# Performance work log

Hardware: AMD Instinct MI355X
Metric: run time of the kernel (lower is better)

Reference implementation:

```python
import jax, jax.numpy as jnp
import numpy as np
from jax.ops import segment_sum, segment_max

N, E = 50000, 800000
F_IN, H, C = 256, 4, 64
HID_LIN, OUT = 128, 16
K = 10
NEG_SLOPE = 0.2


def setup_inputs() -> dict:
    key = jax.random.key(0)
    ks = jax.random.split(key, 16)
    g = lambda k, shape, fan: jax.random.normal(k, shape, jnp.float32) * (1.0 / np.sqrt(fan))
    x = jax.random.normal(ks[0], (N, F_IN), jnp.float32)
    edge_index = jax.random.randint(ks[1], (2, E), 0, N, jnp.int64)
    # conv1: in=F_IN -> H*C, concat=True
    W1 = g(ks[2], (H * C, F_IN), F_IN)
    att_s1 = g(ks[3], (1, H, C), C)
    att_d1 = g(ks[4], (1, H, C), C)
    b1 = jnp.zeros((H * C,), jnp.float32)
    # conv2: in=H*C -> C, concat=False
    W2 = g(ks[5], (H * C, H * C), H * C)
    att_s2 = g(ks[6], (1, H, C), C)
    att_d2 = g(ks[7], (1, H, C), C)
    b2 = jnp.zeros((C,), jnp.float32)
    # linear head: C -> HID_LIN -> OUT
    Wl1 = g(ks[8], (HID_LIN, C), C)
    bl1 = jnp.zeros((HID_LIN,), jnp.float32)
    Wl2 = g(ks[9], (OUT, HID_LIN), HID_LIN)
    bl2 = jnp.zeros((OUT,), jnp.float32)
    return dict(x=x, W1=W1, att_s1=att_s1, att_d1=att_d1, b1=b1,
                W2=W2, att_s2=att_s2, att_d2=att_d2, b2=b2,
                Wl1=Wl1, bl1=bl1, Wl2=Wl2, bl2=bl2, edge_index=edge_index)


def gat_conv(x, edge_index, W, att_s, att_d, bias, concat):
    src, dst = edge_index[0], edge_index[1]
    n = x.shape[0]
    xl = (x @ W.T).reshape(n, H, C)              # [N,H,C]
    a_s = jnp.sum(xl * att_s, axis=-1)           # [N,H]
    a_d = jnp.sum(xl * att_d, axis=-1)           # [N,H]
    alpha = jax.nn.leaky_relu(a_s[src] + a_d[dst], NEG_SLOPE)  # [E,H]

    # per-(dst,head) top-k mask via sort-by-segment (rank within neighborhood)
    e = alpha.shape[0]
    counts = segment_sum(jnp.ones((e,), jnp.int32), dst, num_segments=n)
    start = jnp.cumsum(counts) - counts          # segment start offsets

    def head_mask(a):
        order = jnp.lexsort((-a, dst))           # sort by dst asc, alpha desc
        rank = jnp.arange(e) - start[dst[order]]
        return jnp.zeros((e,), bool).at[order].set(rank < K)

    mask = jax.vmap(head_mask, in_axes=1, out_axes=1)(alpha)  # [E,H]

    # segment softmax over destination with top-k mask (masked -> -inf)
    neg_inf = jnp.finfo(alpha.dtype).min
    a_masked = jnp.where(mask, alpha, neg_inf)
    m = segment_max(a_masked, dst, num_segments=n)            # [N,H]
    ex = jnp.where(mask, jnp.exp(alpha - m[dst]), 0.0)        # alpha<=m on kept edges
    denom = segment_sum(ex, dst, num_segments=n)              # [N,H]
    att = ex / jnp.where(denom[dst] > 0, denom[dst], 1.0)     # [E,H]

    # message + scatter-add aggregation
    out = segment_sum(att[:, :, None] * xl[src], dst, num_segments=n)  # [N,H,C]
    out = out.reshape(n, H * C) if concat else out.mean(axis=1)
    return out + bias


def reference(x, W1, att_s1, att_d1, b1, W2, att_s2, att_d2, b2,
              Wl1, bl1, Wl2, bl2, edge_index):
    h = gat_conv(x, edge_index, W1, att_s1, att_d1, b1, concat=True)
    h = gat_conv(h, edge_index, W2, att_s2, att_d2, b2, concat=False)
    h = jax.nn.relu(h @ Wl1.T + bl1)             # dropout is identity in eval
    return h @ Wl2.T + bl2
```

## Files before the change

kernel.cpp:

```cpp
#include <hip/hip_runtime.h>
#include <math.h>

#define F_IN 256
#define HC   256
#define H_   4
#define C_   64
#define KTOP 10
#define NEG_SLOPE 0.2f

#define BM 128
#define BN 128
#define BK 16
#define LDP (BM + 4)
__global__ __launch_bounds__(256) void gemm_nt(const float* __restrict__ A,
                                               const float* __restrict__ B,
                                               float* __restrict__ Cc,
                                               int M, int K, int No) {
  __shared__ float As[BK][LDP];
  __shared__ float Bs[BK][LDP];
  const int bm = blockIdx.x * BM;
  const int bn = blockIdx.y * BN;
  const int tid = threadIdx.x;
  const int tx = tid & 15, ty = tid >> 4;
  const int lrow = tid >> 1;
  const int lk   = (tid & 1) << 3;
  const bool arow_ok = (bm + lrow < M);
  const float* aptr = A + (size_t)(bm + lrow) * K + lk;
  const float* bptr = B + (size_t)(bn + lrow) * K + lk;
  float acc[8][8] = {};
  for (int k0 = 0; k0 < K; k0 += BK) {
    float4 a0 = make_float4(0.f, 0.f, 0.f, 0.f), a1 = a0;
    if (arow_ok) {
      const float* ap = aptr + k0;
      a0 = *(const float4*)ap;
      a1 = *(const float4*)(ap + 4);
    }
    const float* bp = bptr + k0;
    float4 b0 = *(const float4*)bp;
    float4 b1 = *(const float4*)(bp + 4);
    __syncthreads();
    As[lk + 0][lrow] = a0.x; As[lk + 1][lrow] = a0.y; As[lk + 2][lrow] = a0.z; As[lk + 3][lrow] = a0.w;
    As[lk + 4][lrow] = a1.x; As[lk + 5][lrow] = a1.y; As[lk + 6][lrow] = a1.z; As[lk + 7][lrow] = a1.w;
    Bs[lk + 0][lrow] = b0.x; Bs[lk + 1][lrow] = b0.y; Bs[lk + 2][lrow] = b0.z; Bs[lk + 3][lrow] = b0.w;
    Bs[lk + 4][lrow] = b1.x; Bs[lk + 5][lrow] = b1.y; Bs[lk + 6][lrow] = b1.z; Bs[lk + 7][lrow] = b1.w;
    __syncthreads();
#pragma unroll
    for (int kk = 0; kk < BK; ++kk) {
      float a[8];
      *(float4*)&a[0] = *(const float4*)&As[kk][ty * 8];
      *(float4*)&a[4] = *(const float4*)&As[kk][ty * 8 + 4];
      {
        float4 bv = *(const float4*)&Bs[kk][tx * 4];
#pragma unroll
        for (int i = 0; i < 8; ++i) {
          acc[i][0] += a[i] * bv.x; acc[i][1] += a[i] * bv.y;
          acc[i][2] += a[i] * bv.z; acc[i][3] += a[i] * bv.w;
        }
      }
      {
        float4 bv = *(const float4*)&Bs[kk][64 + tx * 4];
#pragma unroll
        for (int i = 0; i < 8; ++i) {
          acc[i][4] += a[i] * bv.x; acc[i][5] += a[i] * bv.y;
          acc[i][6] += a[i] * bv.z; acc[i][7] += a[i] * bv.w;
        }
      }
    }
  }
#pragma unroll
  for (int i = 0; i < 8; ++i) {
    int r = bm + ty * 8 + i;
    if (r < M) {
      float* cp = Cc + (size_t)r * No + bn;
      *(float4*)(cp + tx * 4) = make_float4(acc[i][0], acc[i][1], acc[i][2], acc[i][3]);
      *(float4*)(cp + 64 + tx * 4) = make_float4(acc[i][4], acc[i][5], acc[i][6], acc[i][7]);
    }
  }
}

__global__ __launch_bounds__(256) void gemm_bias_relu(const float* __restrict__ A,
                                                      const float* __restrict__ B,
                                                      const float* __restrict__ bias,
                                                      float* __restrict__ Cc,
                                                      int M, int K, int No) {
  __shared__ float As[BK][LDP];
  __shared__ float Bs[BK][LDP];
  const int bm = blockIdx.x * BM;
  const int bn = blockIdx.y * BN;
  const int tid = threadIdx.x;
  const int tx = tid & 15, ty = tid >> 4;
  const int lrow = tid >> 1;
  const int lk   = (tid & 1) << 3;
  const bool arow_ok = (bm + lrow < M);
  const bool brow_ok = (bn + lrow < No);
  const float* aptr = A + (size_t)(bm + lrow) * K + lk;
  const float* bptr = B + (size_t)(bn + lrow) * K + lk;
  float acc[8][8] = {};
  for (int k0 = 0; k0 < K; k0 += BK) {
    float4 a0 = make_float4(0.f, 0.f, 0.f, 0.f), a1 = a0, b0 = a0, b1 = a0;
    if (arow_ok) {
      const float* ap = aptr + k0;
      a0 = *(const float4*)ap;
      a1 = *(const float4*)(ap + 4);
    }
    if (brow_ok) {
      const float* bp = bptr + k0;
      b0 = *(const float4*)bp;
      b1 = *(const float4*)(bp + 4);
    }
    __syncthreads();
    As[lk + 0][lrow] = a0.x; As[lk + 1][lrow] = a0.y; As[lk + 2][lrow] = a0.z; As[lk + 3][lrow] = a0.w;
    As[lk + 4][lrow] = a1.x; As[lk + 5][lrow] = a1.y; As[lk + 6][lrow] = a1.z; As[lk + 7][lrow] = a1.w;
    Bs[lk + 0][lrow] = b0.x; Bs[lk + 1][lrow] = b0.y; Bs[lk + 2][lrow] = b0.z; Bs[lk + 3][lrow] = b0.w;
    Bs[lk + 4][lrow] = b1.x; Bs[lk + 5][lrow] = b1.y; Bs[lk + 6][lrow] = b1.z; Bs[lk + 7][lrow] = b1.w;
    __syncthreads();
#pragma unroll
    for (int kk = 0; kk < BK; ++kk) {
      float a[8];
      *(float4*)&a[0] = *(const float4*)&As[kk][ty * 8];
      *(float4*)&a[4] = *(const float4*)&As[kk][ty * 8 + 4];
      {
        float4 bv = *(const float4*)&Bs[kk][tx * 4];
#pragma unroll
        for (int i = 0; i < 8; ++i) {
          acc[i][0] += a[i] * bv.x; acc[i][1] += a[i] * bv.y;
          acc[i][2] += a[i] * bv.z; acc[i][3] += a[i] * bv.w;
        }
      }
      {
        float4 bv = *(const float4*)&Bs[kk][64 + tx * 4];
#pragma unroll
        for (int i = 0; i < 8; ++i) {
          acc[i][4] += a[i] * bv.x; acc[i][5] += a[i] * bv.y;
          acc[i][6] += a[i] * bv.z; acc[i][7] += a[i] * bv.w;
        }
      }
    }
  }
#pragma unroll
  for (int i = 0; i < 8; ++i) {
    int r = bm + ty * 8 + i;
    if (r < M) {
      float* cp = Cc + (size_t)r * No + bn;
#pragma unroll
      for (int j = 0; j < 4; ++j) {
        int col = tx * 4 + j;
        cp[col] = fmaxf(acc[i][j] + bias[bn + col], 0.f);
      }
#pragma unroll
      for (int j = 0; j < 4; ++j) {
        int col = 64 + tx * 4 + j;
        cp[col] = fmaxf(acc[i][4 + j] + bias[bn + col], 0.f);
      }
    }
  }
}

__global__ __launch_bounds__(256) void head_out(const float* __restrict__ hid,
                                                const float* __restrict__ Wl2,
                                                const float* __restrict__ bl2,
                                                float* __restrict__ out, int n_nodes) {
  int t = blockIdx.x * 256 + threadIdx.x;
  int n = t >> 4, o = t & 15;
  if (n >= n_nodes) return;
  const float4* hp = (const float4*)(hid + (size_t)n * 128);
  const float4* wp = (const float4*)(Wl2 + (size_t)o * 128);
  float acc = bl2[o];
#pragma unroll
  for (int k = 0; k < 32; ++k) {
    float4 hv = hp[k], wv = wp[k];
    acc += hv.x * wv.x + hv.y * wv.y + hv.z * wv.z + hv.w * wv.w;
  }
  out[(size_t)n * 16 + o] = acc;
}

__global__ __launch_bounds__(256) void fold_att1(const float* __restrict__ W1,
                                                 const float* __restrict__ att_s,
                                                 const float* __restrict__ att_d,
                                                 double* __restrict__ wt) {
  int t = blockIdx.x * 256 + threadIdx.x;
  if (t >= H_ * HC) return;
  int h = t >> 8;
  int k = t & (HC - 1);
  double s = 0.0, d = 0.0;
#pragma unroll 4
  for (int c = 0; c < C_; ++c) {
    double w = (double)W1[(size_t)(h * C_ + c) * HC + k];
    s += w * (double)att_s[h * C_ + c];
    d += w * (double)att_d[h * C_ + c];
  }
  wt[(size_t)(2 * h + 0) * HC + k] = s;
  wt[(size_t)(2 * h + 1) * HC + k] = d;
}

__global__ __launch_bounds__(256) void fold_att2(const float* __restrict__ W2,
                                                 const float* __restrict__ att_s,
                                                 const float* __restrict__ att_d,
                                                 double* __restrict__ u_s,
                                                 double* __restrict__ u_d) {
  int t = blockIdx.x * 256 + threadIdx.x;
  if (t >= H_ * HC) return;
  int h = t >> 8;
  int k = t & (HC - 1);
  double s = 0.0, d = 0.0;
#pragma unroll 4
  for (int c = 0; c < C_; ++c) {
    double w = (double)W2[(size_t)(h * C_ + c) * HC + k];
    s += w * (double)att_s[h * C_ + c];
    d += w * (double)att_d[h * C_ + c];
  }
  u_s[t] = s;
  u_d[t] = d;
}

__global__ __launch_bounds__(256) void fold_vv(const float* __restrict__ W1,
                                               const double* __restrict__ u2s,
                                               const double* __restrict__ u2d,
                                               const float* __restrict__ b1,
                                               double* __restrict__ wt,
                                               double* __restrict__ cst) {
  int t = blockIdx.x * 256 + threadIdx.x;
  if (t < 8192) {
    int type = t >> 12;
    int rem = t & 4095;
    int j = rem & 255;
    int hh = rem >> 8;
    int h = hh >> 2, hp = hh & 3;
    const double* u2 = type ? u2d : u2s;
    double acc = 0.0;
#pragma unroll 4
    for (int c = 0; c < C_; ++c)
      acc += (double)W1[(size_t)(h * C_ + c) * HC + j] * u2[hp * HC + h * C_ + c];
    wt[(size_t)(8 + type * 16 + hh) * HC + j] = acc;
  } else if (t < 8200) {
    int q = t - 8192;
    const double* u2 = (q >> 2) ? u2d : u2s;
    int hp = q & 3;
    double acc = 0.0;
    for (int k = 0; k < HC; ++k) acc += (double)b1[k] * u2[hp * HC + k];
    cst[q] = acc;
  }
}

#define SNB 128
#define SKB 32
__global__ __launch_bounds__(256) void scores_gemm(const float* __restrict__ x,
                                                   const double* __restrict__ wt,
                                                   double* __restrict__ as1,
                                                   double* __restrict__ ad1,
                                                   double* __restrict__ zz, int n_nodes) {
  __shared__ float  Xs[SNB][SKB + 1];
  __shared__ double Ws[40][SKB + 1];
  const int tid = threadIdx.x;
  const int n0 = blockIdx.x * SNB;
  const int g = tid & 3;
  const int p = tid >> 2;
  double acc0[10] = {}, acc1[10] = {};
  for (int k0 = 0; k0 < HC; k0 += SKB) {
    __syncthreads();
    {
      int row = tid >> 1;
      int colb = (tid & 1) * 16;
      float* d = &Xs[row][colb];
      int n = n0 + row;
      if (n < n_nodes) {
        const float* xp = x + (size_t)n * HC + k0 + colb;
        float4 v0 = *(const float4*)(xp);
        float4 v1 = *(const float4*)(xp + 4);
        float4 v2 = *(const float4*)(xp + 8);
        float4 v3 = *(const float4*)(xp + 12);
        d[0] = v0.x;  d[1] = v0.y;  d[2] = v0.z;  d[3] = v0.w;
        d[4] = v1.x;  d[5] = v1.y;  d[6] = v1.z;  d[7] = v1.w;
        d[8] = v2.x;  d[9] = v2.y;  d[10] = v2.z; d[11] = v2.w;
        d[12] = v3.x; d[13] = v3.y; d[14] = v3.z; d[15] = v3.w;
      } else {
#pragma unroll
        for (int j = 0; j < 16; ++j) d[j] = 0.f;
      }
    }
#pragma unroll
    for (int q = 0; q < 5; ++q) {
      int idx = tid + q * 256;
      int row = idx >> 5, col = idx & 31;
      Ws[row][col] = wt[(size_t)row * HC + k0 + col];
    }
    __syncthreads();
#pragma unroll
    for (int kk = 0; kk < SKB; ++kk) {
      double xv0 = (double)Xs[2 * p][kk];
      double xv1 = (double)Xs[2 * p + 1][kk];
#pragma unroll
      for (int ci = 0; ci < 10; ++ci) {
        double w = Ws[g * 10 + ci][kk];
        acc0[ci] += xv0 * w;
        acc1[ci] += xv1 * w;
      }
    }
  }
  const int na = n0 + 2 * p;
  const int nb = na + 1;
  if (na < n_nodes) {
#pragma unroll
    for (int ci = 0; ci < 10; ++ci) {
      int c = g * 10 + ci;
      double v = acc0[ci];
      if (c < 8)       ((c & 1) ? ad1 : as1)[na * H_ + (c >> 1)] = v;
      else if (c < 24) { int hh = c - 8;  zz[((size_t)na * H_ + (hh >> 2)) * 8 + (hh & 3)] = v; }
      else             { int hh = c - 24; zz[((size_t)na * H_ + (hh >> 2)) * 8 + 4 + (hh & 3)] = v; }
    }
  }
  if (nb < n_nodes) {
#pragma unroll
    for (int ci = 0; ci < 10; ++ci) {
      int c = g * 10 + ci;
      double v = acc1[ci];
      if (c < 8)       ((c & 1) ? ad1 : as1)[nb * H_ + (c >> 1)] = v;
      else if (c < 24) { int hh = c - 8;  zz[((size_t)nb * H_ + (hh >> 2)) * 8 + (hh & 3)] = v; }
      else             { int hh = c - 24; zz[((size_t)nb * H_ + (hh >> 2)) * 8 + 4 + (hh & 3)] = v; }
    }
  }
}

__global__ void count_edges(const int* __restrict__ dst, int E_, int* __restrict__ counts) {
  int e = blockIdx.x * blockDim.x + threadIdx.x;
  if (e < E_) atomicAdd(&counts[dst[e]], 1);
}

#define SCB 256
__global__ __launch_bounds__(SCB) void scan_phase1(const int* __restrict__ counts, int n,
                                                   int* __restrict__ row_start,
                                                   int* __restrict__ bsum) {
  __shared__ int sh[SCB];
  int b = blockIdx.x, t = threadIdx.x;
  int idx = b * SCB + t;
  int v = (idx < n) ? counts[idx] : 0;
  sh[t] = v;
  __syncthreads();
  for (int off = 1; off < SCB; off <<= 1) {
    int u = (t >= off) ? sh[t - off] : 0;
    __syncthreads();
    sh[t] += u;
    __syncthreads();
  }
  if (idx < n) row_start[idx] = sh[t] - v;
  if (t == SCB - 1) bsum[b] = sh[t];
}

__global__ __launch_bounds__(SCB) void scan_phase2(int* __restrict__ bsum, int nb) {
  __shared__ int sh[SCB];
  int t = threadIdx.x;
  int v = (t < nb) ? bsum[t] : 0;
  sh[t] = v;
  __syncthreads();
  for (int off = 1; off < SCB; off <<= 1) {
    int u = (t >= off) ? sh[t - off] : 0;
    __syncthreads();
    sh[t] += u;
    __syncthreads();
  }
  if (t < nb) bsum[t] = sh[t] - v;
}

__global__ __launch_bounds__(SCB) void scan_phase3(int n, const int* __restrict__ bsum,
                                                   int* __restrict__ row_start,
                                                   int* __restrict__ wptr, int E_) {
  int b = blockIdx.x, t = threadIdx.x;
  int idx = b * SCB + t;
  if (idx < n) {
    int r = row_start[idx] + bsum[b];
    row_start[idx] = r;
    wptr[idx] = r;
  } else if (idx == n) {
    row_start[n] = E_;
  }
}

__global__ void scatter_edges(const int* __restrict__ src, const int* __restrict__ dst, int E_,
                              int* __restrict__ wptr, int* __restrict__ csr_src) {
  int e = blockIdx.x * blockDim.x + threadIdx.x;
  if (e < E_) {
    int p = atomicAdd(&wptr[dst[e]], 1);
    csr_src[p] = src[e];
  }
}

__global__ void bin_big(const int* __restrict__ row_start, int n_nodes,
                        int* __restrict__ list64, int* __restrict__ cnt) {
  int n = blockIdx.x * blockDim.x + threadIdx.x;
  if (n >= n_nodes) return;
  int deg = row_start[n + 1] - row_start[n];
  if (deg > 32) { int p = atomicAdd(&cnt[1], 1); list64[p] = n; }
}

__device__ inline unsigned long long shfl_xor_u64(unsigned long long x, int m) {
  int lo = __shfl_xor((int)(x & 0xffffffffull), m);
  int hi = __shfl_xor((int)(x >> 32), m);
  return ((unsigned long long)(unsigned int)hi << 32) | (unsigned int)lo;
}
__device__ inline unsigned long long mono_key(double v) {
  unsigned long long u = (unsigned long long)__double_as_longlong(v);
  return (u & 0x8000000000000000ull) ? ~u : (u | 0x8000000000000000ull);
}
__device__ inline double mono_val(unsigned long long k) {
  unsigned long long u = (k & 0x8000000000000000ull) ? (k ^ 0x8000000000000000ull) : ~k;
  return __longlong_as_double((long long)u);
}

__global__ __launch_bounds__(256) void select32(const double* __restrict__ as_,
                                                const double* __restrict__ ad_,
                                                const int* __restrict__ row_start,
                                                const int* __restrict__ csr_src,
                                                int n_nodes,
                                                int* __restrict__ ksrc,
                                                float* __restrict__ kw,
                                                double* __restrict__ kw64) {
  const int slot = threadIdx.x & 31;
  const int grp  = threadIdx.x >> 5;
  const int nl   = grp >> 2;
  const int h    = grp & 3;
  const int lane = threadIdx.x & 63;
  const int gbase = lane & 32;
  for (int base = blockIdx.x * 2; base < n_nodes; base += gridDim.x * 2) {
    int n = base + nl;
    bool active = (n < n_nodes);
    int nn = active ? n : 0;
    int rs = row_start[nn];
    int deg = active ? (row_start[nn + 1] - rs) : 0;
    if (deg > 32) { active = false; deg = 0; }
    double adv = ad_[nn * H_ + h];
    int kcount = deg < KTOP ? deg : KTOP;

    unsigned long long key; int sv;
    if (slot < deg) {
      int s = csr_src[rs + slot];
      double a = as_[s * H_ + h] + adv;
      double v = (a >= 0.0) ? a : (double)NEG_SLOPE * a;
      key = (mono_key(v) & ~31ull) | (unsigned long long)(31 - slot);
      sv = s;
    } else {
      key = (mono_key(-INFINITY) & ~31ull) | (unsigned long long)(31 - slot);
      sv = -1;
    }
#pragma unroll
    for (int kk = 2; kk <= 32; kk <<= 1) {
#pragma unroll
      for (int j = kk >> 1; j > 0; j >>= 1) {
        unsigned long long ok = shfl_xor_u64(key, j);
        bool dirDesc = ((slot & kk) == 0);
        bool lower   = ((slot & j) == 0);
        bool mineFirst = key > ok;
        if ((dirDesc == lower) ? !mineFirst : mineFirst) key = ok;
      }
    }
    int wslot = 31 - (int)(key & 31ull);
    int sid = __shfl(sv, gbase + wslot);
    double vrec = mono_val(key & ~31ull);
    double m = __shfl(vrec, gbase);
    double ex = (slot < kcount) ? exp(vrec - m) : 0.0;
    double den = ex;
#pragma unroll
    for (int off = 16; off >= 1; off >>= 1) den += __shfl_xor(den, off);
    double inv = (kcount > 0) ? 1.0 / den : 0.0;
    double wgt = ex * inv;

    if (active && slot < KTOP) {
      size_t u = ((size_t)n * H_ + h) * KTOP + slot;
      ksrc[u] = (sid >= 0) ? sid : 0;
      kw[u] = (float)wgt;
      if (kw64) kw64[u] = wgt;
    }
  }
}

__global__ __launch_bounds__(256) void select64(const double* __restrict__ as_,
                                                const double* __restrict__ ad_,
                                                const int* __restrict__ row_start,
                                                const int* __restrict__ csr_src,
                                                const int* __restrict__ list,
                                                const int* __restrict__ cnt,
                                                int* __restrict__ ksrc,
                                                float* __restrict__ kw,
                                                double* __restrict__ kw64) {
  __shared__ int    f_src[H_][16];
  __shared__ double f_w[H_][16];
  const int c = cnt[1];
  int h = threadIdx.x >> 6;
  int lane = threadIdx.x & 63;
  for (int idx = blockIdx.x; idx < c; idx += gridDim.x) {
    int n = list[idx];
    int rs = row_start[n];
    int deg = row_start[n + 1] - rs;
    if (deg > 256) deg = 256;
    double adv = ad_[n * H_ + h];
    int kcount = deg < KTOP ? deg : KTOP;

    double vsel; int sid;
    if (deg <= 64) {
      unsigned long long key; int sv;
      if (lane < deg) {
        int s = csr_src[rs + lane];
        double a = as_[s * H_ + h] + adv;
        double v = (a >= 0.0) ? a : (double)NEG_SLOPE * a;
        key = (mono_key(v) & ~63ull) | (unsigned long long)(63 - lane);
        sv = s;
      } else {
        key = (mono_key(-INFINITY) & ~63ull) | (unsigned long long)(63 - lane);
        sv = -1;
      }
#pragma unroll
      for (int kk = 2; kk <= 64; kk <<= 1) {
#pragma unroll
        for (int j = kk >> 1; j > 0; j >>= 1) {
          unsigned long long ok = shfl_xor_u64(key, j);
          bool dirDesc = ((lane & kk) == 0);
          bool lower   = ((lane & j) == 0);
          bool mineFirst = key > ok;
          if ((dirDesc == lower) ? !mineFirst : mineFirst) key = ok;
        }
      }
      int wslot = 63 - (int)(key & 63ull);
      sid = __shfl(sv, wslot);
      vsel = mono_val(key & ~63ull);
    } else {
      double av[4]; int svr[4];
#pragma unroll
      for (int q = 0; q < 4; ++q) {
        int id2 = lane + (q << 6);
        if (id2 < deg) {
          int s = csr_src[rs + id2];
          double a = as_[s * H_ + h] + adv;
          av[q] = (a >= 0.0) ? a : (double)NEG_SLOPE * a;
          svr[q] = s;
        } else {
          av[q] = -INFINITY; svr[q] = -1;
        }
      }
      for (int it = 0; it < kcount; ++it) {
        double best = av[0]; int bq = 0;
#pragma unroll
        for (int q = 1; q < 4; ++q)
          if (av[q] > best) { best = av[q]; bq = q; }
        double bv = best; int bl = lane;
#pragma unroll
        for (int off = 32; off >= 1; off >>= 1) {
          double ov = __shfl_down(bv, off);
          int    ol = __shfl_down(bl, off);
          if (ov > bv || (ov == bv && ol < bl)) { bv = ov; bl = ol; }
        }
        bl = __shfl(bl, 0);
        if (lane == bl) {
          f_src[h][it] = svr[bq];
          f_w[h][it] = best;
          av[bq] = -INFINITY;
        }
      }
      vsel = (lane < kcount) ? f_w[h][lane] : -INFINITY;
      sid  = (lane < kcount) ? f_src[h][lane] : -1;
    }

    double m = __shfl(vsel, 0);
    double ex = (lane < kcount) ? exp(vsel - m) : 0.0;
    double den = ex;
#pragma unroll
    for (int off = 32; off >= 1; off >>= 1) den += __shfl_xor(den, off);
    double inv = (kcount > 0) ? 1.0 / den : 0.0;
    double wgt = ex * inv;

    if (lane < KTOP) {
      size_t u = ((size_t)n * H_ + h) * KTOP + lane;
      ksrc[u] = (sid >= 0) ? sid : 0;
      kw[u] = (float)wgt;
      if (kw64) kw64[u] = wgt;
    }
  }
}

__global__ __launch_bounds__(256) void conv2_scores(const int* __restrict__ ksrc,
                                                    const double* __restrict__ kw64,
                                                    const double* __restrict__ zz,
                                                    const double* __restrict__ cst,
                                                    double* __restrict__ as2,
                                                    double* __restrict__ ad2, int n_nodes) {
  int n = (blockIdx.x * 256 + threadIdx.x) >> 6;
  int lane = threadIdx.x & 63;
  if (n >= n_nodes) return;
  int p = lane >> 3, j = lane & 7;
  const int*    sp = ksrc + (size_t)n * H_ * KTOP;
  const double* wp = kw64 + (size_t)n * H_ * KTOP;
  double acc = 0.0;
#pragma unroll
  for (int t = 0; t < 5; ++t) {
    int q = j + t * 8;
    int h = q / KTOP;
    double w = wp[q];
    int s = sp[q];
    acc += w * zz[((size_t)s * H_ + h) * 8 + p];
  }
#pragma unroll
  for (int off = 4; off >= 1; off >>= 1) acc += __shfl_xor(acc, off);
  if (j == 0) {
    double vo = acc + cst[p];
    if (p < 4) as2[n * H_ + p] = vo;
    else       ad2[n * H_ + (p - 4)] = vo;
  }
}

template <int CONCAT>
__global__ __launch_bounds__(256) void gather_agg(const float* __restrict__ xl,
                                                  const int* __restrict__ ksrc,
                                                  const float* __restrict__ kw,
                                                  const float* __restrict__ bias,
                                                  float* __restrict__ out, int n_nodes) {
  int n = (blockIdx.x * 256 + threadIdx.x) >> 6;
  int lane = threadIdx.x & 63;
  if (n >= n_nodes) return;
  const int*   sp = ksrc + (size_t)n * H_ * KTOP;
  const float* wp = kw   + (size_t)n * H_ * KTOP;
  int ss[H_ * KTOP];
#pragma unroll
  for (int k = 0; k < H_ * KTOP; ++k) ss[k] = sp[k];
  float xv[H_ * KTOP];
#pragma unroll
  for (int h = 0; h < H_; ++h)
#pragma unroll
    for (int i = 0; i < KTOP; ++i)
      xv[h * KTOP + i] = xl[(size_t)ss[h * KTOP + i] * HC + h * C_ + lane];
  float accs[H_];
#pragma unroll
  for (int h = 0; h < H_; ++h) {
    float a = 0.f;
#pragma unroll
    for (int i = 0; i < KTOP; ++i) a += wp[h * KTOP + i] * xv[h * KTOP + i];
    accs[h] = a;
  }
  if (CONCAT) {
#pragma unroll
    for (int h = 0; h < H_; ++h)
      out[(size_t)n * HC + h * C_ + lane] = accs[h] + bias[h * C_ + lane];
  } else {
    out[(size_t)n * C_ + lane] =
        0.25f * (accs[0] + accs[1] + accs[2] + accs[3]) + bias[lane];
  }
}

extern "C" void kernel_launch(void* const* d_in, const int* in_sizes, int n_in,
                              void* d_out, int out_size, void* d_ws, size_t ws_size,
                              hipStream_t stream) {
  const float* x      = (const float*)d_in[0];
  const float* W1     = (const float*)d_in[1];
  const float* att_s1 = (const float*)d_in[2];
  const float* att_d1 = (const float*)d_in[3];
  const float* b1     = (const float*)d_in[4];
  const float* W2     = (const float*)d_in[5];
  const float* att_s2 = (const float*)d_in[6];
  const float* att_d2 = (const float*)d_in[7];
  const float* b2     = (const float*)d_in[8];
  const float* Wl1    = (const float*)d_in[9];
  const float* bl1    = (const float*)d_in[10];
  const float* Wl2    = (const float*)d_in[11];
  const float* bl2    = (const float*)d_in[12];
  const int*   eidx   = (const int*)d_in[13];

  const int N_ = in_sizes[0] / F_IN;
  const int E_ = in_sizes[13] / 2;
  const int* e_src = eidx;
  const int* e_dst = eidx + E_;

  char* base = (char*)d_ws;
  size_t off = 0;
  auto alloc = [&](size_t bytes) -> char* {
    char* p = base + off;
    off = (off + bytes + 255) & ~(size_t)255;
    return p;
  };
  float*  xl        = (float*)alloc((size_t)N_ * HC * 4);
  float*  hbuf      = (float*)alloc((size_t)N_ * HC * 4);
  double* as1       = (double*)alloc((size_t)N_ * H_ * 8);
  double* ad1       = (double*)alloc((size_t)N_ * H_ * 8);
  double* as2       = (double*)alloc((size_t)N_ * H_ * 8);
  double* ad2       = (double*)alloc((size_t)N_ * H_ * 8);
  double* zz        = (double*)alloc((size_t)N_ * H_ * 8 * 8);
  double* wt        = (double*)alloc((size_t)40 * HC * 8);
  double* u2s       = (double*)alloc((size_t)H_ * HC * 8);
  double* u2d       = (double*)alloc((size_t)H_ * HC * 8);
  double* cst       = (double*)alloc((size_t)8 * 8);
  int*    ksrc1     = (int*)alloc((size_t)N_ * H_ * KTOP * 4);
  float*  kw1       = (float*)alloc((size_t)N_ * H_ * KTOP * 4);
  double* kw64_1    = (double*)alloc((size_t)N_ * H_ * KTOP * 8);
  int*    ksrc2     = (int*)alloc((size_t)N_ * H_ * KTOP * 4);
  float*  kw2       = (float*)alloc((size_t)N_ * H_ * KTOP * 4);
  int*    list64    = (int*)alloc((size_t)N_ * 4);
  int*    cnt       = (int*)alloc((size_t)8 * 4);
  int*    bsum      = (int*)alloc((size_t)SCB * 4);
  int* counts       = (int*)alloc((size_t)N_ * 4);
  int* row_start    = (int*)alloc((size_t)(N_ + 1) * 4);
  int* wptr         = (int*)alloc((size_t)N_ * 4);
  int* csr_src      = (int*)alloc((size_t)E_ * 4);
  (void)ws_size;
  float* hidbuf  = xl;

  const int eb = (E_ + 255) / 256;
  const int nb = (N_ + 255) / 256;
  const int sb = (N_ + 1 + SCB - 1) / SCB;

  hipMemsetAsync(counts, 0, (size_t)N_ * 4, stream);
  hipMemsetAsync(cnt, 0, 32, stream);
  count_edges<<<eb, 256, 0, stream>>>(e_dst, E_, counts);
  scan_phase1<<<sb, SCB, 0, stream>>>(counts, N_, row_start, bsum);
  scan_phase2<<<1, SCB, 0, stream>>>(bsum, sb);
  scan_phase3<<<sb, SCB, 0, stream>>>(N_, bsum, row_start, wptr, E_);
  scatter_edges<<<eb, 256, 0, stream>>>(e_src, e_dst, E_, wptr, csr_src);
  bin_big<<<nb, 256, 0, stream>>>(row_start, N_, list64, cnt);

  fold_att1<<<(H_ * HC + 255) / 256, 256, 0, stream>>>(W1, att_s1, att_d1, wt);
  fold_att2<<<(H_ * HC + 255) / 256, 256, 0, stream>>>(W2, att_s2, att_d2, u2s, u2d);
  fold_vv<<<(8200 + 255) / 256, 256, 0, stream>>>(W1, u2s, u2d, b1, wt, cst);
  scores_gemm<<<(N_ + SNB - 1) / SNB, 256, 0, stream>>>(x, wt, as1, ad1, zz, N_);

  dim3 ggrid((N_ + BM - 1) / BM, HC / BN);
  gemm_nt<<<ggrid, 256, 0, stream>>>(x, W1, xl, N_, F_IN, HC);

  select32<<<6250, 256, 0, stream>>>(as1, ad1, row_start, csr_src, N_, ksrc1, kw1, kw64_1);
  select64<<<1024, 256, 0, stream>>>(as1, ad1, row_start, csr_src, list64, cnt,
                                     ksrc1, kw1, kw64_1);
  conv2_scores<<<(N_ + 3) / 4, 256, 0, stream>>>(ksrc1, kw64_1, zz, cst, as2, ad2, N_);

  select32<<<6250, 256, 0, stream>>>(as2, ad2, row_start, csr_src, N_, ksrc2, kw2, nullptr);
  select64<<<1024, 256, 0, stream>>>(as2, ad2, row_start, csr_src, list64, cnt,
                                     ksrc2, kw2, nullptr);

  const int agg_blocks = (N_ + 3) / 4;

  gather_agg<1><<<agg_blocks, 256, 0, stream>>>(xl, ksrc1, kw1, b1, hbuf, N_);

  gemm_nt<<<ggrid, 256, 0, stream>>>(hbuf, W2, xl, N_, HC, HC);
  gather_agg<0><<<agg_blocks, 256, 0, stream>>>(xl, ksrc2, kw2, b2, hbuf, N_);

  dim3 hgrid((N_ + BM - 1) / BM, 1);
  gemm_bias_relu<<<hgrid, 256, 0, stream>>>(hbuf, Wl1, bl1, hidbuf, N_, C_, 128);
  head_out<<<(N_ * 16 + 255) / 256, 256, 0, stream>>>(hidbuf, Wl2, bl2, (float*)d_out, N_);
}
```

Before: 825.6 us.

## Replace FP32 SIMT GEMM with split-bf16 MFMA GEMM for GAT projections

Both dense projection GEMMs (x@W1^T and h@W2^T) now use a matrix-core kernel. Each fp32 operand is split into high and low bf16 parts, and three bf16 MFMA products are accumulated to approximate fp32 precision. The goal is to move the FLOP-heavy GEMMs off the scalar FMA path onto MFMA units. The cost is conversion work during staging and extra LDS traffic. Output stores are now scalar and strided instead of float4, and the dropped low×low term slightly reduces accuracy.

```diff
diff --git a/kernel.cpp b/kernel.cpp
--- a/kernel.cpp
+++ b/kernel.cpp
@@ -8,76 +8,116 @@
 #define KTOP 10
 #define NEG_SLOPE 0.2f
 
+typedef __attribute__((ext_vector_type(8))) short bf16x8;
+typedef __attribute__((ext_vector_type(4))) float f32x4;
+
+#define GM 128
+#define GN 128
+#define GK 32
+__device__ inline unsigned short f2bf_rn(float f) {
+  unsigned u = __float_as_uint(f);
+  unsigned r = u + 0x7FFFu + ((u >> 16) & 1u);
+  return (unsigned short)(r >> 16);
+}
+__global__ __launch_bounds__(256) void gemm_nt_mfma(const float* __restrict__ A,
+                                                    const float* __restrict__ B,
+                                                    float* __restrict__ Cc,
+                                                    int M, int K, int No) {
+  __shared__ unsigned short Ah[4][128][8], Al[4][128][8];
+  __shared__ unsigned short Bh[4][128][8], Bl[4][128][8];
+  const int tid = threadIdx.x;
+  const int bm = blockIdx.x * GM, bn = blockIdx.y * GN;
+  const int r = tid >> 1, half = tid & 1;
+  const int wid = tid >> 6, lane = tid & 63;
+  const int wr = wid >> 1, wc = wid & 1;
+  const int qp = lane >> 4, fr = lane & 15;
+  const bool arow_ok = (bm + r < M);
+  const float* ap = A + (size_t)(bm + r) * K + half * 16;
+  const float* bp = B + (size_t)(bn + r) * K + half * 16;
+  f32x4 acc[4][4];
+#pragma unroll
+  for (int i = 0; i < 4; ++i)
+#pragma unroll
+    for (int j = 0; j < 4; ++j) acc[i][j] = (f32x4){0.f, 0.f, 0.f, 0.f};
+
+  for (int k0 = 0; k0 < K; k0 += GK) {
+    float va[16], vb[16];
+    if (arow_ok) {
+      *(float4*)&va[0]  = *(const float4*)(ap + k0);
+      *(float4*)&va[4]  = *(const float4*)(ap + k0 + 4);
+      *(float4*)&va[8]  = *(const float4*)(ap + k0 + 8);
+      *(float4*)&va[12] = *(const float4*)(ap + k0 + 12);
+    } else {
+#pragma unroll
+      for (int j = 0; j < 16; ++j) va[j] = 0.f;
+    }
+    *(float4*)&vb[0]  = *(const float4*)(bp + k0);
+    *(float4*)&vb[4]  = *(const float4*)(bp + k0 + 4);
+    *(float4*)&vb[8]  = *(const float4*)(bp + k0 + 8);
+    *(float4*)&vb[12] = *(const float4*)(bp + k0 + 12);
+    __syncthreads();
+#pragma unroll
+    for (int c = 0; c < 4; ++c) {
+      ushort4 ha, la, hb, lb;
+      {
+        float f0 = va[c * 4 + 0], f1 = va[c * 4 + 1], f2 = va[c * 4 + 2], f3 = va[c * 4 + 3];
+        ha.x = f2bf_rn(f0); ha.y = f2bf_rn(f1); ha.z = f2bf_rn(f2); ha.w = f2bf_rn(f3);
+        la.x = f2bf_rn(f0 - __uint_as_float((unsigned)ha.x << 16));
+        la.y = f2bf_rn(f1 - __uint_as_float((unsigned)ha.y << 16));
+        la.z = f2bf_rn(f2 - __uint_as_float((unsigned)ha.z << 16));
+        la.w = f2bf_rn(f3 - __uint_as_float((unsigned)ha.w << 16));
+      }
+      {
+        float f0 = vb[c * 4 + 0], f1 = vb[c * 4 + 1], f2 = vb[c * 4 + 2], f3 = vb[c * 4 + 3];
+        hb.x = f2bf_rn(f0); hb.y = f2bf_rn(f1); hb.z = f2bf_rn(f2); hb.w = f2bf_rn(f3);
+        lb.x = f2bf_rn(f0 - __uint_as_float((unsigned)hb.x << 16));
+        lb.y = f2bf_rn(f1 - __uint_as_float((unsigned)hb.y << 16));
+        lb.z = f2bf_rn(f2 - __uint_as_float((unsigned)hb.z << 16));
+        lb.w = f2bf_rn(f3 - __uint_as_float((unsigned)hb.w << 16));
+      }
+      *(ushort4*)&Ah[c][r][half * 4] = ha;
+      *(ushort4*)&Al[c][r][half * 4] = la;
+      *(ushort4*)&Bh[c][r][half * 4] = hb;
+      *(ushort4*)&Bl[c][r][half * 4] = lb;
+    }
+    __syncthreads();
+    bf16x8 bhf[4], blf[4];
+#pragma unroll
+    for (int j = 0; j < 4; ++j) {
+      bhf[j] = *(const bf16x8*)&Bh[qp][wc * 64 + j * 16 + fr][0];
+      blf[j] = *(const bf16x8*)&Bl[qp][wc * 64 + j * 16 + fr][0];
+    }
+#pragma unroll
+    for (int i = 0; i < 4; ++i) {
+      bf16x8 ahf = *(const bf16x8*)&Ah[qp][wr * 64 + i * 16 + fr][0];
+      bf16x8 alf = *(const bf16x8*)&Al[qp][wr * 64 + i * 16 + fr][0];
+#pragma unroll
+      for (int j = 0; j < 4; ++j) {
+        acc[i][j] = __builtin_amdgcn_mfma_f32_16x16x32_bf16(ahf, bhf[j], acc[i][j], 0, 0, 0);
+        acc[i][j] = __builtin_amdgcn_mfma_f32_16x16x32_bf16(ahf, blf[j], acc[i][j], 0, 0, 0);
+        acc[i][j] = __builtin_amdgcn_mfma_f32_16x16x32_bf16(alf, bhf[j], acc[i][j], 0, 0, 0);
+      }
+    }
+  }
+#pragma unroll
+  for (int i = 0; i < 4; ++i) {
+    int row0 = bm + wr * 64 + i * 16 + qp * 4;
+#pragma unroll
+    for (int j = 0; j < 4; ++j) {
+      int col = bn + wc * 64 + j * 16 + fr;
+#pragma unroll
+      for (int t = 0; t < 4; ++t) {
+        int row = row0 + t;
+        if (row < M) Cc[(size_t)row * No + col] = acc[i][j][t];
+      }
+    }
+  }
+}
+
 #define BM 128
 #define BN 128
 #define BK 16
 #define LDP (BM + 4)
-__global__ __launch_bounds__(256) void gemm_nt(const float* __restrict__ A,
-                                               const float* __restrict__ B,
-                                               float* __restrict__ Cc,
-                                               int M, int K, int No) {
-  __shared__ float As[BK][LDP];
-  __shared__ float Bs[BK][LDP];
-  const int bm = blockIdx.x * BM;
-  const int bn = blockIdx.y * BN;
-  const int tid = threadIdx.x;
-  const int tx = tid & 15, ty = tid >> 4;
-  const int lrow = tid >> 1;
-  const int lk   = (tid & 1) << 3;
-  const bool arow_ok = (bm + lrow < M);
-  const float* aptr = A + (size_t)(bm + lrow) * K + lk;
-  const float* bptr = B + (size_t)(bn + lrow) * K + lk;
-  float acc[8][8] = {};
-  for (int k0 = 0; k0 < K; k0 += BK) {
-    float4 a0 = make_float4(0.f, 0.f, 0.f, 0.f), a1 = a0;
-    if (arow_ok) {
-      const float* ap = aptr + k0;
-      a0 = *(const float4*)ap;
-      a1 = *(const float4*)(ap + 4);
-    }
-    const float* bp = bptr + k0;
-    float4 b0 = *(const float4*)bp;
-    float4 b1 = *(const float4*)(bp + 4);
-    __syncthreads();
-    As[lk + 0][lrow] = a0.x; As[lk + 1][lrow] = a0.y; As[lk + 2][lrow] = a0.z; As[lk + 3][lrow] = a0.w;
-    As[lk + 4][lrow] = a1.x; As[lk + 5][lrow] = a1.y; As[lk + 6][lrow] = a1.z; As[lk + 7][lrow] = a1.w;
-    Bs[lk + 0][lrow] = b0.x; Bs[lk + 1][lrow] = b0.y; Bs[lk + 2][lrow] = b0.z; Bs[lk + 3][lrow] = b0.w;
-    Bs[lk + 4][lrow] = b1.x; Bs[lk + 5][lrow] = b1.y; Bs[lk + 6][lrow] = b1.z; Bs[lk + 7][lrow] = b1.w;
-    __syncthreads();
-#pragma unroll
-    for (int kk = 0; kk < BK; ++kk) {
-      float a[8];
-      *(float4*)&a[0] = *(const float4*)&As[kk][ty * 8];
-      *(float4*)&a[4] = *(const float4*)&As[kk][ty * 8 + 4];
-      {
-        float4 bv = *(const float4*)&Bs[kk][tx * 4];
-#pragma unroll
-        for (int i = 0; i < 8; ++i) {
-          acc[i][0] += a[i] * bv.x; acc[i][1] += a[i] * bv.y;
-          acc[i][2] += a[i] * bv.z; acc[i][3] += a[i] * bv.w;
-        }
-      }
-      {
-        float4 bv = *(const float4*)&Bs[kk][64 + tx * 4];
-#pragma unroll
-        for (int i = 0; i < 8; ++i) {
-          acc[i][4] += a[i] * bv.x; acc[i][5] += a[i] * bv.y;
-          acc[i][6] += a[i] * bv.z; acc[i][7] += a[i] * bv.w;
-        }
-      }
-    }
-  }
-#pragma unroll
-  for (int i = 0; i < 8; ++i) {
-    int r = bm + ty * 8 + i;
-    if (r < M) {
-      float* cp = Cc + (size_t)r * No + bn;
-      *(float4*)(cp + tx * 4) = make_float4(acc[i][0], acc[i][1], acc[i][2], acc[i][3]);
-      *(float4*)(cp + 64 + tx * 4) = make_float4(acc[i][4], acc[i][5], acc[i][6], acc[i][7]);
-    }
-  }
-}
-
 __global__ __launch_bounds__(256) void gemm_bias_relu(const float* __restrict__ A,
                                                       const float* __restrict__ B,
                                                       const float* __restrict__ bias,
@@ -717,8 +757,8 @@
   fold_vv<<<(8200 + 255) / 256, 256, 0, stream>>>(W1, u2s, u2d, b1, wt, cst);
   scores_gemm<<<(N_ + SNB - 1) / SNB, 256, 0, stream>>>(x, wt, as1, ad1, zz, N_);
 
-  dim3 ggrid((N_ + BM - 1) / BM, HC / BN);
-  gemm_nt<<<ggrid, 256, 0, stream>>>(x, W1, xl, N_, F_IN, HC);
+  dim3 ggrid((N_ + GM - 1) / GM, HC / GN);
+  gemm_nt_mfma<<<ggrid, 256, 0, stream>>>(x, W1, xl, N_, F_IN, HC);
 
   select32<<<6250, 256, 0, stream>>>(as1, ad1, row_start, csr_src, N_, ksrc1, kw1, kw64_1);
   select64<<<1024, 256, 0, stream>>>(as1, ad1, row_start, csr_src, list64, cnt,
@@ -733,7 +773,7 @@
 
   gather_agg<1><<<agg_blocks, 256, 0, stream>>>(xl, ksrc1, kw1, b1, hbuf, N_);
 
-  gemm_nt<<<ggrid, 256, 0, stream>>>(hbuf, W2, xl, N_, HC, HC);
+  gemm_nt_mfma<<<ggrid, 256, 0, stream>>>(hbuf, W2, xl, N_, HC, HC);
   gather_agg<0><<<agg_blocks, 256, 0, stream>>>(xl, ksrc2, kw2, b2, hbuf, N_);
 
   dim3 hgrid((N_ + BM - 1) / BM, 1);
```

New measurement: 716.8 us. 1.15x faster.
